# Kernel tuning notes

Measured on AMD Instinct MI355X. Metric: run time of the kernel, lower is better.

The kernel has to match this reference:

```python
import jax, jax.numpy as jnp
import numpy as np

B, CIN, H, W = 64, 3, 96, 96
COUT, KH, KW = 96, 5, 5
STRIDE, PAD = 2, 2
LR, K_TOP, DELTA, P_LEB = 0.02, 2, -0.4, 3.0
PREC = 1e-30


def im2col(x):
    # torch nn.Unfold ordering: channel-major (C, kh, kw) flattened -> [B, C*KH*KW, L]
    xp = jnp.pad(x, ((0, 0), (0, 0), (PAD, PAD), (PAD, PAD)))
    Hout = (H + 2 * PAD - KH) // STRIDE + 1
    Wout = (W + 2 * PAD - KW) // STRIDE + 1
    cols = []
    for i in range(KH):  # small fixed kernel loop (25 slices)
        for j in range(KW):
            cols.append(xp[:, :, i:i + STRIDE * (Hout - 1) + 1:STRIDE,
                           j:j + STRIDE * (Wout - 1) + 1:STRIDE])
    patches = jnp.stack(cols, axis=2)  # [B, C, KH*KW, Hout, Wout]
    return patches.reshape(x.shape[0], CIN * KH * KW, Hout * Wout)  # [B, K, L]


def setup_inputs() -> dict:
    key = jax.random.key(0)
    k1, k2 = jax.random.split(key)
    inp = jax.random.normal(k1, (B, CIN, H, W), dtype=jnp.float32)
    weight = jax.random.normal(k2, (COUT, CIN, KH, KW), dtype=jnp.float32)  # init.normal_
    return {"input": inp, "weight": weight}


def reference(input, weight):
    # standard conv forward (F.conv2d, no bias)
    out = jax.lax.conv_general_dilated(
        input, weight, (STRIDE, STRIDE), [(PAD, PAD), (PAD, PAD)],
        dimension_numbers=("NCHW", "OIHW", "NCHW"))

    # --- Krotov-Hopfield Hebbian update ---
    pre = im2col(input)                      # [B, K, L]
    Wm = weight.reshape(COUT, -1)            # [O, K]
    # sign(W) * |W|^(p-1) @ pre
    tot = jnp.einsum("ok,bkl->bol", jnp.sign(Wm) * jnp.abs(Wm) ** (P_LEB - 1.0), pre)  # [B,O,L]

    Bn, _, L = tot.shape
    _, idx = jax.lax.top_k(tot.transpose(0, 2, 1), K_TOP)   # [B, L, k] over output channels
    vals = jnp.concatenate([jnp.ones((1,), tot.dtype),
                            jnp.full((K_TOP - 1,), DELTA, tot.dtype)])  # top-1 -> 1.0, rest -> delta
    act = jnp.zeros((Bn, L, COUT), tot.dtype).at[
        jnp.arange(Bn)[:, None, None], jnp.arange(L)[None, :, None], idx
    ].set(jnp.broadcast_to(vals, (Bn, L, K_TOP)))
    act = act.transpose(0, 2, 1)             # [B, O, L]

    yx = jnp.einsum("bol,bkl->ok", act, pre) / L          # mean over L, sum over batch
    yy = (act * tot).sum(0).mean(1)                        # [O]
    ds = yx - yy[:, None] * Wm                             # [O, K]
    nc = jnp.maximum(jnp.max(jnp.abs(ds)), PREC)
    new_weight = weight + LR * (ds / nc).reshape(weight.shape)
    return out, new_weight
```

## Files before the change

### kernel.cpp

```cpp
#include <hip/hip_runtime.h>

#define B_     64
#define HW_    96
#define COUT_  96
#define KK_    75
#define KP_    76
#define KPAD   96
#define HOUT_  48
#define L_     2304
#define LR_    0.02f
#define DELTA_ -0.4f
#define OUT_ELEMS (B_*COUT_*L_)
#define CL2    256
#define CPB2   3
#define NPART2 (B_*3)
#define PROW2  (COUT_*96 + COUT_)
#define CPI    144

typedef __attribute__((ext_vector_type(8))) short short8v;
typedef __attribute__((ext_vector_type(4))) float float4v;
typedef __attribute__((ext_vector_type(4))) unsigned uint4v;

__device__ __forceinline__ unsigned short f2bf(float f) {
  unsigned u = __float_as_uint(f);
  u += 0x7fff + ((u >> 16) & 1);
  return (unsigned short)(u >> 16);
}

__device__ __forceinline__ void ins2(float v, int o, float& v1, int& o1,
                                     float& v2, int& o2) {
  bool b1 = (v > v1) || (v == v1 && o < o1);
  bool b2 = (v > v2) || (v == v2 && o < o2);
  if (b1)      { v2 = v1; o2 = o1; v1 = v; o1 = o; }
  else if (b2) { v2 = v;  o2 = o; }
}

__device__ __forceinline__ void im2col_load(const float* __restrict__ xb, int l,
                                            float* __restrict__ pre) {
  const int oh = l / HOUT_, ow = l - oh * HOUT_;
  #pragma unroll
  for (int c = 0; c < 3; ++c) {
    #pragma unroll
    for (int i = 0; i < 5; ++i) {
      int ih = oh * 2 + i - 2;
      bool okh = ((unsigned)ih < (unsigned)HW_);
      #pragma unroll
      for (int j = 0; j < 5; ++j) {
        int iw = ow * 2 + j - 2;
        float v = 0.0f;
        if (okh && ((unsigned)iw < (unsigned)HW_)) v = xb[(c * HW_ + ih) * HW_ + iw];
        pre[c * 25 + i * 5 + j] = v;
      }
    }
  }
  pre[KK_] = 0.0f;
}

__global__ __launch_bounds__(256) void k0_prep(const float* __restrict__ w,
                                               unsigned short* __restrict__ wbf) {
  int i = blockIdx.x * 256 + threadIdx.x;
  if (i >= 192 * KPAD) return;
  int row = i / KPAD, k = i - row * KPAD;
  float v = 0.0f;
  if (k < KK_) {
    float ww = w[(row % COUT_) * KK_ + k];
    v = (row < COUT_) ? ww : ww * fabsf(ww);
  }
  wbf[i] = f2bf(v);
}

__global__ __launch_bounds__(256, 4) void k1_mfma(
    const float* __restrict__ x, const unsigned short* __restrict__ wbf,
    float* __restrict__ out, float4* __restrict__ top2)
{
  const int tid = threadIdx.x;
  const int lane = tid & 63, wq = tid >> 6;
  const int gid = blockIdx.x * 4 + wq;
  const int b = gid / CPI;
  const int chunk = gid - b * CPI;
  const int l0 = chunk * 16;
  const int col = lane & 15, g = lane >> 4;
  const float* xb = x + (size_t)b * (3 * HW_ * HW_);

  const int l = l0 + col;
  const int oh = l / HOUT_, ow = l - oh * HOUT_;
  const int ihb = 2 * oh - 2, iwb = 2 * ow - 2;

  short8v bfr[3];
  #pragma unroll
  for (int kt = 0; kt < 3; ++kt) {
    uint4v pk;
    #pragma unroll
    for (int e2 = 0; e2 < 4; ++e2) {
      float v0 = 0.0f, v1 = 0.0f;
      const int k0 = kt * 32 + g * 8 + 2 * e2;
      if (k0 < KK_) {
        int c = k0 / 25, r = k0 - 25 * c, ki = r / 5, kj = r - 5 * ki;
        int ih = ihb + ki, iw = iwb + kj;
        if ((unsigned)ih < (unsigned)HW_ && (unsigned)iw < (unsigned)HW_)
          v0 = xb[(c * HW_ + ih) * HW_ + iw];
      }
      const int k1e = k0 + 1;
      if (k1e < KK_) {
        int c = k1e / 25, r = k1e - 25 * c, ki = r / 5, kj = r - 5 * ki;
        int ih = ihb + ki, iw = iwb + kj;
        if ((unsigned)ih < (unsigned)HW_ && (unsigned)iw < (unsigned)HW_)
          v1 = xb[(c * HW_ + ih) * HW_ + iw];
      }
      pk[e2] = (unsigned)f2bf(v0) | ((unsigned)f2bf(v1) << 16);
    }
    bfr[kt] = __builtin_bit_cast(short8v, pk);
  }

  float4v acc[12];
  #pragma unroll
  for (int mt = 0; mt < 12; ++mt) acc[mt] = (float4v)(0.0f);
  #pragma unroll
  for (int kt = 0; kt < 3; ++kt) {
    #pragma unroll
    for (int mt = 0; mt < 12; ++mt) {
      short8v afr = *(const short8v*)(
          wbf + ((mt * 16 + col) * KPAD + kt * 32 + g * 8));
      acc[mt] = __builtin_amdgcn_mfma_f32_16x16x32_bf16(
          afr, bfr[kt], acc[mt], 0, 0, 0);
    }
  }

  #pragma unroll
  for (int mt = 0; mt < 6; ++mt) {
    #pragma unroll
    for (int r = 0; r < 4; ++r) {
      const int ch = mt * 16 + g * 4 + r;
      out[((size_t)b * COUT_ + ch) * L_ + l0 + col] = acc[mt][r];
    }
  }

  float v1 = -3.0e38f, v2 = -3.0e38f;
  int o1 = 0x7fffffff, o2 = 0x7fffffff;
  #pragma unroll
  for (int mt = 6; mt < 12; ++mt)
    #pragma unroll
    for (int r = 0; r < 4; ++r)
      ins2(acc[mt][r], (mt - 6) * 16 + g * 4 + r, v1, o1, v2, o2);
  #pragma unroll
  for (int st = 0; st < 2; ++st) {
    const int d = (st == 0) ? 16 : 32;
    float bv1 = __shfl_xor(v1, d, 64);
    int   bo1 = __shfl_xor(o1, d, 64);
    float bv2 = __shfl_xor(v2, d, 64);
    int   bo2 = __shfl_xor(o2, d, 64);
    ins2(bv1, bo1, v1, o1, v2, o2);
    ins2(bv2, bo2, v1, o1, v2, o2);
  }
  if (g == 0)
    top2[(size_t)b * L_ + l0 + col] =
        make_float4(v1, __int_as_float(o1), v2, __int_as_float(o2));
}

__global__ __launch_bounds__(256, 1) void k2_gemm(
    const float* __restrict__ x, const float4* __restrict__ top2,
    float* __restrict__ part)
{
  __shared__ __align__(16) unsigned short actS[COUT_ * CL2];
  __shared__ __align__(16) unsigned short preT[COUT_ * CL2];
  __shared__ float yyS[COUT_];
  const int tid = threadIdx.x;
  const int b = blockIdx.y;
  const int pos = tid;
  const float* xb = x + (size_t)b * (3 * HW_ * HW_);

  {
    float4* a4 = (float4*)actS;
    float4* p4 = (float4*)preT;
    #pragma unroll
    for (int i = 0; i < 12; ++i) {
      a4[tid + i * 256] = make_float4(0, 0, 0, 0);
      p4[tid + i * 256] = make_float4(0, 0, 0, 0);
    }
    if (tid < COUT_) yyS[tid] = 0.0f;
  }
  __syncthreads();

  const int lane = tid & 63, w = tid >> 6;
  const int col = lane & 15, g = lane >> 4;
  const int mb = (w >> 1) * 48, nb = (w & 1) * 48;

  float4v acc[3][3];
  #pragma unroll
  for (int mt = 0; mt < 3; ++mt)
    #pragma unroll
    for (int nt = 0; nt < 3; ++nt) acc[mt][nt] = (float4v)(0.0f);

  int prevA = -1, prevB = -1;

  for (int ch = 0; ch < CPB2; ++ch) {
    const int l0 = (blockIdx.x * CPB2 + ch) * CL2;
    if (prevA >= 0) {
      *(unsigned short*)((char*)actS + prevA) = 0;
      *(unsigned short*)((char*)actS + prevB) = 0;
    }
    {
      float pre[KP_];
      im2col_load(xb, l0 + pos, pre);
      const int pblk = pos >> 3, plo = (pos & 7) << 1;
      #pragma unroll
      for (int k = 0; k < KK_; ++k) {
        int byteoff = k * 512 + ((pblk ^ (k & 7)) << 4) + plo;
        *(unsigned short*)((char*)preT + byteoff) = f2bf(pre[k]);
      }
      float4 t2 = top2[(size_t)b * L_ + l0 + pos];
      int o1 = __float_as_int(t2.y), o2 = __float_as_int(t2.w);
      prevA = o1 * 512 + ((pblk ^ (o1 & 7)) << 4) + plo;
      prevB = o2 * 512 + ((pblk ^ (o2 & 7)) << 4) + plo;
      *(unsigned short*)((char*)actS + prevA) = 0x3F80;
      *(unsigned short*)((char*)actS + prevB) = f2bf(DELTA_);
      atomicAdd(&yyS[o1], t2.x);
      atomicAdd(&yyS[o2], DELTA_ * t2.z);
    }
    __syncthreads();

    #pragma unroll
    for (int kt = 0; kt < 8; ++kt) {
      short8v a[3], bf[3];
      #pragma unroll
      for (int mt = 0; mt < 3; ++mt) {
        int row = mb + mt * 16 + col;
        a[mt] = *(const short8v*)((char*)actS + row * 512 +
                                  (((kt * 4 + g) ^ (row & 7)) << 4));
      }
      #pragma unroll
      for (int nt = 0; nt < 3; ++nt) {
        int row = nb + nt * 16 + col;
        bf[nt] = *(const short8v*)((char*)preT + row * 512 +
                                   (((kt * 4 + g) ^ (row & 7)) << 4));
      }
      #pragma unroll
      for (int mt = 0; mt < 3; ++mt)
        #pragma unroll
        for (int nt = 0; nt < 3; ++nt)
          acc[mt][nt] = __builtin_amdgcn_mfma_f32_16x16x32_bf16(
              a[mt], bf[nt], acc[mt][nt], 0, 0, 0);
    }
    __syncthreads();
  }

  float* prow = part + (size_t)(b * 3 + blockIdx.x) * PROW2;
  #pragma unroll
  for (int mt = 0; mt < 3; ++mt)
    #pragma unroll
    for (int nt = 0; nt < 3; ++nt)
      #pragma unroll
      for (int r = 0; r < 4; ++r) {
        int m = mb + mt * 16 + g * 4 + r;
        int n = nb + nt * 16 + col;
        prow[m * 96 + n] = acc[mt][nt][r];
      }
  if (tid < COUT_) prow[9216 + tid] = yyS[tid];
}

__global__ __launch_bounds__(256) void k3_reduce(
    const float* __restrict__ part, float* __restrict__ finals)
{
  __shared__ float red[4][64];
  const int e = blockIdx.x * 64 + (threadIdx.x & 63);
  const int seg = threadIdx.x >> 6;
  float s = 0.0f;
  if (e < PROW2)
    for (int p = seg * (NPART2 / 4); p < (seg + 1) * (NPART2 / 4); ++p)
      s += part[(size_t)p * PROW2 + e];
  red[seg][threadIdx.x & 63] = s;
  __syncthreads();
  if (seg == 0 && e < PROW2) {
    int ll = threadIdx.x & 63;
    float t = (red[0][ll] + red[1][ll]) + (red[2][ll] + red[3][ll]);
    if (e < 9216) {
      int o = e / 96, kw = e - o * 96;
      if (kw < KK_) finals[o * KK_ + kw] = t;
    } else {
      finals[COUT_ * KK_ + (e - 9216)] = t;
    }
  }
}

__global__ __launch_bounds__(256) void k4_finalize(
    const float* __restrict__ w, const float* __restrict__ finals,
    float* __restrict__ outw)
{
  __shared__ float dsS[COUT_ * KK_];
  __shared__ float wmax[4];
  __shared__ float ncS;
  const int tid = threadIdx.x;
  float m = 0.0f;
  for (int i = tid; i < COUT_ * KK_; i += 256) {
    int o = i / KK_;
    float d = finals[i] - finals[COUT_ * KK_ + o] * w[i];
    dsS[i] = d;
    m = fmaxf(m, fabsf(d));
  }
  #pragma unroll
  for (int s = 32; s > 0; s >>= 1) m = fmaxf(m, __shfl_xor(m, s, 64));
  if ((tid & 63) == 0) wmax[tid >> 6] = m;
  __syncthreads();
  if (tid == 0) {
    float n = fmaxf(fmaxf(wmax[0], wmax[1]), fmaxf(wmax[2], wmax[3]));
    ncS = fmaxf(n, 1e-30f);
  }
  __syncthreads();
  const float scale = LR_ / ncS;
  for (int i = tid; i < COUT_ * KK_; i += 256) {
    outw[i] = w[i] + scale * dsS[i];
  }
}

extern "C" void kernel_launch(void* const* d_in, const int* in_sizes, int n_in,
                              void* d_out, int out_size, void* d_ws, size_t ws_size,
                              hipStream_t stream) {
  (void)in_sizes; (void)n_in; (void)out_size; (void)ws_size;
  const float* x = (const float*)d_in[0];
  const float* w = (const float*)d_in[1];
  float* out  = (float*)d_out;
  float* outw = out + OUT_ELEMS;

  unsigned short* wbf = (unsigned short*)d_ws;
  float4* top2 = (float4*)((char*)d_ws + 192 * KPAD * 2);
  float*  part = (float*)((char*)top2 + (size_t)B_ * L_ * sizeof(float4));
  float*  finals = part + (size_t)NPART2 * PROW2;

  k0_prep   <<<dim3((192 * KPAD + 255) / 256), 256, 0, stream>>>(w, wbf);
  k1_mfma   <<<dim3(B_ * CPI / 4), 256, 0, stream>>>(x, wbf, out, top2);
  k2_gemm   <<<dim3(3, B_), 256, 0, stream>>>(x, top2, part);
  k3_reduce <<<dim3((PROW2 + 63) / 64), 256, 0, stream>>>(part, finals);
  k4_finalize<<<dim3(1), 256, 0, stream>>>(w, finals, outw);
}
```

Measured before the change: 116.0 us.

## Stage conv output through LDS for coalesced stores and split Hebbian GEMM wider

k1 now launches with a 2D grid where each block covers 64 contiguous output positions of one batch image. It transposes its conv results through a shared-memory tile so that each wave writes 64 contiguous floats per channel row using nontemporal stores, replacing the earlier scattered 16-wide stores. k2 drops the 3-chunk loop and runs 9 blocks per batch, one 256-position chunk each, which triples the grid and removes the act-tile reset. Partial rows are packed at 75 columns instead of 96, so the reduction handles more partials with simpler indexing. The cost is more partial buffers to sum in k3, plus extra LDS and a barrier in k1.

```diff
diff --git a/kernel.cpp b/kernel.cpp
--- a/kernel.cpp
+++ b/kernel.cpp
@@ -12,10 +12,8 @@
 #define DELTA_ -0.4f
 #define OUT_ELEMS (B_*COUT_*L_)
 #define CL2    256
-#define CPB2   3
-#define NPART2 (B_*3)
-#define PROW2  (COUT_*96 + COUT_)
-#define CPI    144
+#define NPART  (B_*9)
+#define ROW    (COUT_*KK_ + COUT_)
 
 typedef __attribute__((ext_vector_type(8))) short short8v;
 typedef __attribute__((ext_vector_type(4))) float float4v;
@@ -73,16 +71,15 @@
     const float* __restrict__ x, const unsigned short* __restrict__ wbf,
     float* __restrict__ out, float4* __restrict__ top2)
 {
+  __shared__ float cT[COUT_][68];
   const int tid = threadIdx.x;
   const int lane = tid & 63, wq = tid >> 6;
-  const int gid = blockIdx.x * 4 + wq;
-  const int b = gid / CPI;
-  const int chunk = gid - b * CPI;
-  const int l0 = chunk * 16;
+  const int b = blockIdx.y;
+  const int bl0 = blockIdx.x * 64;
   const int col = lane & 15, g = lane >> 4;
   const float* xb = x + (size_t)b * (3 * HW_ * HW_);
 
-  const int l = l0 + col;
+  const int l = bl0 + wq * 16 + col;
   const int oh = l / HOUT_, ow = l - oh * HOUT_;
   const int ihb = 2 * oh - 2, iwb = 2 * ow - 2;
 
@@ -127,13 +124,10 @@
   }
 
   #pragma unroll
-  for (int mt = 0; mt < 6; ++mt) {
-    #pragma unroll
-    for (int r = 0; r < 4; ++r) {
-      const int ch = mt * 16 + g * 4 + r;
-      out[((size_t)b * COUT_ + ch) * L_ + l0 + col] = acc[mt][r];
-    }
-  }
+  for (int mt = 0; mt < 6; ++mt)
+    #pragma unroll
+    for (int r = 0; r < 4; ++r)
+      cT[mt * 16 + g * 4 + r][wq * 16 + col] = acc[mt][r];
 
   float v1 = -3.0e38f, v2 = -3.0e38f;
   int o1 = 0x7fffffff, o2 = 0x7fffffff;
@@ -153,8 +147,17 @@
     ins2(bv2, bo2, v1, o1, v2, o2);
   }
   if (g == 0)
-    top2[(size_t)b * L_ + l0 + col] =
+    top2[(size_t)b * L_ + l] =
         make_float4(v1, __int_as_float(o1), v2, __int_as_float(o2));
+
+  __syncthreads();
+
+  #pragma unroll
+  for (int it = 0; it < 24; ++it) {
+    const int ch = wq * 24 + it;
+    __builtin_nontemporal_store(
+        cT[ch][lane], &out[((size_t)b * COUT_ + ch) * L_ + bl0 + lane]);
+  }
 }
 
 __global__ __launch_bounds__(256, 1) void k2_gemm(
@@ -181,6 +184,27 @@
   }
   __syncthreads();
 
+  const int l0 = blockIdx.x * CL2;
+  {
+    float pre[KP_];
+    im2col_load(xb, l0 + pos, pre);
+    const int pblk = pos >> 3, plo = (pos & 7) << 1;
+    #pragma unroll
+    for (int k = 0; k < KK_; ++k) {
+      int byteoff = k * 512 + ((pblk ^ (k & 7)) << 4) + plo;
+      *(unsigned short*)((char*)preT + byteoff) = f2bf(pre[k]);
+    }
+    float4 t2 = top2[(size_t)b * L_ + l0 + pos];
+    int o1 = __float_as_int(t2.y), o2 = __float_as_int(t2.w);
+    *(unsigned short*)((char*)actS + o1 * 512 + ((pblk ^ (o1 & 7)) << 4) + plo)
+        = 0x3F80;
+    *(unsigned short*)((char*)actS + o2 * 512 + ((pblk ^ (o2 & 7)) << 4) + plo)
+        = f2bf(DELTA_);
+    atomicAdd(&yyS[o1], t2.x);
+    atomicAdd(&yyS[o2], DELTA_ * t2.z);
+  }
+  __syncthreads();
+
   const int lane = tid & 63, w = tid >> 6;
   const int col = lane & 15, g = lane >> 4;
   const int mb = (w >> 1) * 48, nb = (w & 1) * 48;
@@ -191,60 +215,31 @@
     #pragma unroll
     for (int nt = 0; nt < 3; ++nt) acc[mt][nt] = (float4v)(0.0f);
 
-  int prevA = -1, prevB = -1;
-
-  for (int ch = 0; ch < CPB2; ++ch) {
-    const int l0 = (blockIdx.x * CPB2 + ch) * CL2;
-    if (prevA >= 0) {
-      *(unsigned short*)((char*)actS + prevA) = 0;
-      *(unsigned short*)((char*)actS + prevB) = 0;
-    }
-    {
-      float pre[KP_];
-      im2col_load(xb, l0 + pos, pre);
-      const int pblk = pos >> 3, plo = (pos & 7) << 1;
+  #pragma unroll
+  for (int kt = 0; kt < 8; ++kt) {
+    short8v a[3], bf[3];
+    #pragma unroll
+    for (int mt = 0; mt < 3; ++mt) {
+      int row = mb + mt * 16 + col;
+      a[mt] = *(const short8v*)((char*)actS + row * 512 +
+                                (((kt * 4 + g) ^ (row & 7)) << 4));
+    }
+    #pragma unroll
+    for (int nt = 0; nt < 3; ++nt) {
+      int row = nb + nt * 16 + col;
+      bf[nt] = *(const short8v*)((char*)preT + row * 512 +
+                                 (((kt * 4 + g) ^ (row & 7)) << 4));
+    }
+    #pragma unroll
+    for (int mt = 0; mt < 3; ++mt)
       #pragma unroll
-      for (int k = 0; k < KK_; ++k) {
-        int byteoff = k * 512 + ((pblk ^ (k & 7)) << 4) + plo;
-        *(unsigned short*)((char*)preT + byteoff) = f2bf(pre[k]);
-      }
-      float4 t2 = top2[(size_t)b * L_ + l0 + pos];
-      int o1 = __float_as_int(t2.y), o2 = __float_as_int(t2.w);
-      prevA = o1 * 512 + ((pblk ^ (o1 & 7)) << 4) + plo;
-      prevB = o2 * 512 + ((pblk ^ (o2 & 7)) << 4) + plo;
-      *(unsigned short*)((char*)actS + prevA) = 0x3F80;
-      *(unsigned short*)((char*)actS + prevB) = f2bf(DELTA_);
-      atomicAdd(&yyS[o1], t2.x);
-      atomicAdd(&yyS[o2], DELTA_ * t2.z);
-    }
-    __syncthreads();
-
-    #pragma unroll
-    for (int kt = 0; kt < 8; ++kt) {
-      short8v a[3], bf[3];
-      #pragma unroll
-      for (int mt = 0; mt < 3; ++mt) {
-        int row = mb + mt * 16 + col;
-        a[mt] = *(const short8v*)((char*)actS + row * 512 +
-                                  (((kt * 4 + g) ^ (row & 7)) << 4));
-      }
-      #pragma unroll
-      for (int nt = 0; nt < 3; ++nt) {
-        int row = nb + nt * 16 + col;
-        bf[nt] = *(const short8v*)((char*)preT + row * 512 +
-                                   (((kt * 4 + g) ^ (row & 7)) << 4));
-      }
-      #pragma unroll
-      for (int mt = 0; mt < 3; ++mt)
-        #pragma unroll
-        for (int nt = 0; nt < 3; ++nt)
-          acc[mt][nt] = __builtin_amdgcn_mfma_f32_16x16x32_bf16(
-              a[mt], bf[nt], acc[mt][nt], 0, 0, 0);
-    }
-    __syncthreads();
-  }
-
-  float* prow = part + (size_t)(b * 3 + blockIdx.x) * PROW2;
+      for (int nt = 0; nt < 3; ++nt)
+        acc[mt][nt] = __builtin_amdgcn_mfma_f32_16x16x32_bf16(
+            a[mt], bf[nt], acc[mt][nt], 0, 0, 0);
+  }
+  __syncthreads();
+
+  float* prow = part + (size_t)(b * 9 + blockIdx.x) * ROW;
   #pragma unroll
   for (int mt = 0; mt < 3; ++mt)
     #pragma unroll
@@ -253,9 +248,9 @@
       for (int r = 0; r < 4; ++r) {
         int m = mb + mt * 16 + g * 4 + r;
         int n = nb + nt * 16 + col;
-        prow[m * 96 + n] = acc[mt][nt][r];
+        if (n < KK_) prow[m * KK_ + n] = acc[mt][nt][r];
       }
-  if (tid < COUT_) prow[9216 + tid] = yyS[tid];
+  if (tid < COUT_) prow[COUT_ * KK_ + tid] = yyS[tid];
 }
 
 __global__ __launch_bounds__(256) void k3_reduce(
@@ -265,20 +260,13 @@
   const int e = blockIdx.x * 64 + (threadIdx.x & 63);
   const int seg = threadIdx.x >> 6;
   float s = 0.0f;
-  if (e < PROW2)
-    for (int p = seg * (NPART2 / 4); p < (seg + 1) * (NPART2 / 4); ++p)
-      s += part[(size_t)p * PROW2 + e];
+  for (int p = seg * (NPART / 4); p < (seg + 1) * (NPART / 4); ++p)
+    s += part[(size_t)p * ROW + e];
   red[seg][threadIdx.x & 63] = s;
   __syncthreads();
-  if (seg == 0 && e < PROW2) {
+  if (seg == 0) {
     int ll = threadIdx.x & 63;
-    float t = (red[0][ll] + red[1][ll]) + (red[2][ll] + red[3][ll]);
-    if (e < 9216) {
-      int o = e / 96, kw = e - o * 96;
-      if (kw < KK_) finals[o * KK_ + kw] = t;
-    } else {
-      finals[COUT_ * KK_ + (e - 9216)] = t;
-    }
+    finals[e] = (red[0][ll] + red[1][ll]) + (red[2][ll] + red[3][ll]);
   }
 }
 
@@ -324,11 +312,11 @@
   unsigned short* wbf = (unsigned short*)d_ws;
   float4* top2 = (float4*)((char*)d_ws + 192 * KPAD * 2);
   float*  part = (float*)((char*)top2 + (size_t)B_ * L_ * sizeof(float4));
-  float*  finals = part + (size_t)NPART2 * PROW2;
+  float*  finals = part + (size_t)NPART * ROW;
 
   k0_prep   <<<dim3((192 * KPAD + 255) / 256), 256, 0, stream>>>(w, wbf);
-  k1_mfma   <<<dim3(B_ * CPI / 4), 256, 0, stream>>>(x, wbf, out, top2);
-  k2_gemm   <<<dim3(3, B_), 256, 0, stream>>>(x, top2, part);
-  k3_reduce <<<dim3((PROW2 + 63) / 64), 256, 0, stream>>>(part, finals);
+  k1_mfma   <<<dim3(L_ / 64, B_), 256, 0, stream>>>(x, wbf, out, top2);
+  k2_gemm   <<<dim3(9, B_), 256, 0, stream>>>(x, top2, part);
+  k3_reduce <<<dim3(ROW / 64), 256, 0, stream>>>(part, finals);
   k4_finalize<<<dim3(1), 256, 0, stream>>>(w, finals, outw);
 }
```

New measurement: 128.3 us. +10.6%, slower.
